# Performance work log

Hardware: AMD Instinct MI355X
Metric: run time of the kernel (lower is better)

The kernel has to match this reference:

```python
import jax, jax.numpy as jnp
import numpy as np

DIM = 1024
HEADS = 16


def setup_inputs() -> dict:
    key = jax.random.key(0)
    ks = jax.random.split(key, 9)
    B, N, C = 2, 2048, DIM
    hd = C // HEADS
    s = 1.0 / np.sqrt(C)
    x = jax.random.normal(ks[0], (B, N, C), dtype=jnp.float32)
    wq = jax.random.normal(ks[1], (C, C), dtype=jnp.float32) * s
    wk = jax.random.normal(ks[2], (C, C), dtype=jnp.float32) * s
    wv = jax.random.normal(ks[3], (C, C), dtype=jnp.float32) * s
    wp = jax.random.normal(ks[4], (C, C), dtype=jnp.float32) * s
    bp = jnp.zeros((C,), dtype=jnp.float32)
    # rotary table: angles theta_j = 10000^{-2j/hd}, positions 0..N-1
    inv_freq = 1.0 / (10000.0 ** (jnp.arange(0, hd, 2, dtype=jnp.float32) / hd))
    ang = jnp.arange(N, dtype=jnp.float32)[:, None] * inv_freq[None, :]  # (N, hd//2)
    cos = jnp.cos(ang)
    sin = jnp.sin(ang)
    return {"x": x, "wq": wq, "wk": wk, "wv": wv, "wp": wp, "bp": bp,
            "cos": cos, "sin": sin, "num_heads": HEADS}


def _apply_rotary(t, cos, sin):
    # t: (B, N, H, D); cos/sin: (N, D//2) -> broadcast (1, N, 1, D//2)
    B, N, H, D = t.shape
    tr = t.reshape(B, N, H, D // 2, 2)
    t1, t2 = tr[..., 0], tr[..., 1]
    c = cos[None, :, None, :]
    s = sin[None, :, None, :]
    o1 = t1 * c - t2 * s
    o2 = t1 * s + t2 * c
    return jnp.stack([o1, o2], axis=-1).reshape(B, N, H, D)


def reference(x, wq, wk, wv, wp, bp, cos, sin, num_heads):
    B, N, C = x.shape
    H = num_heads
    D = C // H
    q = (x @ wq.T).reshape(B, N, H, D)
    k = (x @ wk.T).reshape(B, N, H, D)
    v = (x @ wv.T).reshape(B, N, H, D)
    q = _apply_rotary(q, cos, sin)
    k = _apply_rotary(k, cos, sin)
    scale = 1.0 / jnp.sqrt(jnp.asarray(D, dtype=x.dtype))
    # scores: (B, H, N, N)
    scores = jnp.einsum('bnhd,bmhd->bhnm', q, k) * scale
    attn = jax.nn.softmax(scores, axis=-1)
    out = jnp.einsum('bhnm,bmhd->bnhd', attn, v).reshape(B, N, C)
    return out @ wp.T + bp
```

## Files before the change

### kernel.cpp

```cpp
#include <hip/hip_runtime.h>
#include <hip/hip_bf16.h>
#include <stdint.h>

#define DEVI __device__ __forceinline__

using bf16 = __hip_bfloat16;
typedef __bf16 bf16x8 __attribute__((ext_vector_type(8)));
typedef __bf16 bf16x4 __attribute__((ext_vector_type(4)));
typedef float f32x4 __attribute__((ext_vector_type(4)));

static constexpr int Bb = 2, Nn = 2048, Cc = 1024, Hh = 16, Dd = 64;
static constexpr float CSC = 0.125f * 1.44269504088896340736f;

DEVI bf16 f2bf(float x) {
  __bf16 h = (__bf16)x;
  return *(bf16*)&h;
}
DEVI float fexp2(float x) { return __builtin_amdgcn_exp2f(x); }

DEVI bf16x8 cvt8(f32x4 a, f32x4 b) {
  bf16x8 r;
  r[0] = (__bf16)a[0]; r[1] = (__bf16)a[1]; r[2] = (__bf16)a[2]; r[3] = (__bf16)a[3];
  r[4] = (__bf16)b[0]; r[5] = (__bf16)b[1]; r[6] = (__bf16)b[2]; r[7] = (__bf16)b[3];
  return r;
}

DEVI void gld_lds16(const bf16* g, bf16* l) {
  __builtin_amdgcn_global_load_lds(
      (__attribute__((address_space(1))) void*)(g),
      (__attribute__((address_space(3))) void*)(l),
      16, 0, 0);
}

__global__ __launch_bounds__(256) void k_cvt(const float* __restrict__ x,
                                             const float* __restrict__ wq,
                                             const float* __restrict__ wk,
                                             const float* __restrict__ wv,
                                             const float* __restrict__ wp,
                                             bf16* xb, bf16* wqb, bf16* wkb,
                                             bf16* wvb, bf16* wpb) {
  int bid = blockIdx.x;
  const float* src; bf16* dst; size_t off;
  if (bid < 2048) {
    src = x; dst = xb; off = (size_t)bid * 2048;
  } else {
    int s = (bid - 2048) >> 9, r = (bid - 2048) & 511;
    off = (size_t)r * 2048;
    src = s == 0 ? wq : s == 1 ? wk : s == 2 ? wv : wp;
    dst = s == 0 ? wqb : s == 1 ? wkb : s == 2 ? wvb : wpb;
  }
  size_t i = off + (size_t)threadIdx.x * 8;
  f32x4 a = *(const f32x4*)(src + i);
  f32x4 b = *(const f32x4*)(src + i + 4);
  *(bf16x8*)(dst + i) = cvt8(a, b);
}

template <int MFC, class Epi>
DEVI void gemm_lds_body(const bf16* __restrict__ A, const bf16* __restrict__ Bw,
                        int K, int m0, int n0, bf16* lA, bf16* lB, Epi epi) {
  constexpr int BM = MFC * 32;
  constexpr int PA = BM / 32;
  const int t = threadIdx.x;
  const int lane = t & 63, wave = t >> 6;
  const int wr = wave >> 1, wc = wave & 1;

  f32x4 acc[MFC][4] = {};

  for (int k0 = 0; k0 < K; k0 += 64) {
    __syncthreads();
#pragma unroll
    for (int p = 0; p < PA; ++p) {
      int c = p * 256 + t;
      int row = c >> 3, cis = (c & 7) ^ (row & 7);
      gld_lds16(A + (size_t)(m0 + row) * K + k0 + cis * 8,
                lA + (size_t)(p * 256 + wave * 64) * 8);
    }
#pragma unroll
    for (int p = 0; p < 4; ++p) {
      int c = p * 256 + t;
      int row = c >> 3, cis = (c & 7) ^ (row & 7);
      gld_lds16(Bw + (size_t)(n0 + row) * K + k0 + cis * 8,
                lB + (size_t)(p * 256 + wave * 64) * 8);
    }
    __syncthreads();

#pragma unroll
    for (int kk = 0; kk < 2; ++kk) {
      bf16x8 aF[MFC];
#pragma unroll
      for (int mf = 0; mf < MFC; ++mf) {
        int row = wr * (BM / 2) + mf * 16 + (lane & 15);
        aF[mf] = *(const bf16x8*)(lA + ((row * 64 + kk * 32 + (lane >> 4) * 8) ^ ((row & 7) << 3)));
      }
#pragma unroll
      for (int nf = 0; nf < 4; ++nf) {
        int row = wc * 64 + nf * 16 + (lane & 15);
        bf16x8 bF = *(const bf16x8*)(lB + ((row * 64 + kk * 32 + (lane >> 4) * 8) ^ ((row & 7) << 3)));
#pragma unroll
        for (int mf = 0; mf < MFC; ++mf)
          acc[mf][nf] = __builtin_amdgcn_mfma_f32_16x16x32_bf16(aF[mf], bF, acc[mf][nf], 0, 0, 0);
      }
    }
  }

#pragma unroll
  for (int mf = 0; mf < MFC; ++mf)
#pragma unroll
    for (int nf = 0; nf < 4; ++nf)
#pragma unroll
      for (int r = 0; r < 4; ++r) {
        int gm = m0 + wr * (BM / 2) + mf * 16 + (lane >> 4) * 4 + r;
        int gn = n0 + wc * 64 + nf * 16 + (lane & 15);
        epi(gm, gn, acc[mf][nf][r]);
      }
}

struct EpiRope {
  bf16* dst; const float* cosw; const float* sinw; float scale;
  DEVI void operator()(int gm, int gn, float v) const {
    int b = gm >> 11, n = gm & 2047;
    int h = gn >> 6, d = gn & 63;
    int i = d >> 1;
    float c = cosw[n * 32 + i], s = sinw[n * 32 + i];
    float p = __shfl_xor(v, 1);
    float o = (d & 1) ? (p * s + v * c) : (v * c - p * s);
    dst[((size_t)(b * Hh + h) * Nn + n) * 64 + d] = f2bf(o * scale);
  }
};

struct EpiVt {
  bf16* dst;
  DEVI void operator()(int gm, int gn, float v) const {
    int h = gm >> 6, d = gm & 63;
    int b = gn >> 11, n = gn & 2047;
    dst[((size_t)(b * Hh + h) * 64 + d) * Nn + n] = f2bf(v);
  }
};

struct EpiProj {
  float* dst; const float* bias;
  DEVI void operator()(int gm, int gn, float v) const {
    dst[(size_t)gm * Cc + gn] = v + bias[gn];
  }
};

__global__ __launch_bounds__(256) void k_qkv(const bf16* __restrict__ xb,
                                             const bf16* __restrict__ wqb,
                                             const bf16* __restrict__ wkb,
                                             const bf16* __restrict__ wvb,
                                             bf16* q_ws, bf16* k_ws, bf16* vt_ws,
                                             const float* __restrict__ cw,
                                             const float* __restrict__ sw) {
  __shared__ __align__(16) bf16 smem[2 * 128 * 64];
  bf16* lA = smem;
  bf16* lB = smem + 128 * 64;
  int bid = blockIdx.x;
  if (bid < 512) {
    int sub = bid & 255;
    int m0 = (sub >> 3) * 128, n0 = (sub & 7) * 128;
    bool isq = bid < 256;
    gemm_lds_body<4>(xb, isq ? wqb : wkb, Cc, m0, n0, lA, lB,
                     EpiRope{isq ? q_ws : k_ws, cw, sw, isq ? CSC : 1.0f});
  } else {
    int sub = bid - 512;
    int m0 = (sub & 7) * 128, n0 = (sub >> 3) * 128;
    gemm_lds_body<4>(wvb, xb, Cc, m0, n0, lA, lB, EpiVt{vt_ws});
  }
}

__global__ __launch_bounds__(256) void k_proj(const bf16* __restrict__ A,
                                              const bf16* __restrict__ W,
                                              float* dst, const float* __restrict__ bias) {
  __shared__ __align__(16) bf16 smem[64 * 64 + 128 * 64];
  gemm_lds_body<2>(A, W, Cc, blockIdx.x * 64, blockIdx.y * 128,
                   smem, smem + 64 * 64, EpiProj{dst, bias});
}

__global__ __launch_bounds__(256) void k_flash(const bf16* __restrict__ q_ws,
                                               const bf16* __restrict__ k_ws,
                                               const bf16* __restrict__ vt_ws,
                                               bf16* __restrict__ attn_o) {
  __shared__ __align__(16) bf16 lK[2][64 * 64];
  __shared__ __align__(16) bf16 lV[2][64 * 64];
  __shared__ __align__(16) bf16 pbuf[4][32 * 64];

  const int t = threadIdx.x, lane = t & 63, wave = t >> 6;
  const int g = lane >> 4;
  const int bh = blockIdx.y;
  const int q0 = blockIdx.x * 128 + wave * 32;
  const bf16* qg = q_ws + (size_t)bh * Nn * 64;
  const bf16* kg = k_ws + (size_t)bh * Nn * 64;
  const bf16* vg = vt_ws + (size_t)bh * 64 * Nn;

  bf16x8 qF[2][2];
#pragma unroll
  for (int qs = 0; qs < 2; ++qs)
#pragma unroll
    for (int kd = 0; kd < 2; ++kd)
      qF[qs][kd] = *(const bf16x8*)(qg + (size_t)(q0 + qs * 16 + (lane & 15)) * 64 + kd * 32 + g * 8);

  f32x4 accO[2][4] = {};
  float LsL[2] = {0.f, 0.f};

  auto stage_tile = [&](int kt, int buf) {
#pragma unroll
    for (int p = 0; p < 2; ++p) {
      int c = p * 256 + t;
      int row = c >> 3, cis = (c & 7) ^ (row & 7);
      bf16* dst = (bf16*)((p * 256 + wave * 64) * 8);
      gld_lds16(kg + (size_t)(kt * 64 + row) * 64 + cis * 8,
                lK[buf] + (size_t)(p * 256 + wave * 64) * 8);
      gld_lds16(vg + (size_t)row * Nn + kt * 64 + cis * 8,
                lV[buf] + (size_t)(p * 256 + wave * 64) * 8);
      (void)dst;
    }
  };

  stage_tile(0, 0);
  __syncthreads();

  constexpr int NT = Nn / 64;
  for (int kt = 0; kt < NT; ++kt) {
    const int cur = kt & 1;
    if (kt + 1 < NT) stage_tile(kt + 1, cur ^ 1);

    f32x4 accT[2][4];
    __builtin_amdgcn_s_setprio(1);
#pragma unroll
    for (int nf = 0; nf < 4; ++nf) {
      int row = nf * 16 + (lane & 15);
      bf16x8 kF0 = *(const bf16x8*)(lK[cur] + ((row * 64 + 0 * 32 + g * 8) ^ ((row & 7) << 3)));
      bf16x8 kF1 = *(const bf16x8*)(lK[cur] + ((row * 64 + 1 * 32 + g * 8) ^ ((row & 7) << 3)));
#pragma unroll
      for (int qs = 0; qs < 2; ++qs) {
        f32x4 sacc = {};
        sacc = __builtin_amdgcn_mfma_f32_16x16x32_bf16(kF0, qF[qs][0], sacc, 0, 0, 0);
        sacc = __builtin_amdgcn_mfma_f32_16x16x32_bf16(kF1, qF[qs][1], sacc, 0, 0, 0);
        accT[qs][nf] = sacc;
      }
    }
    __builtin_amdgcn_s_setprio(0);

#pragma unroll
    for (int qs = 0; qs < 2; ++qs) {
      int prow = qs * 16 + (lane & 15);
      float ps = 0.f;
#pragma unroll
      for (int nf = 0; nf < 4; ++nf) {
        bf16x4 pk;
#pragma unroll
        for (int r = 0; r < 4; ++r) {
          float pv = fexp2(accT[qs][nf][r]);
          ps += pv;
          pk[r] = (__bf16)pv;
        }
        int idx = (prow * 64 + nf * 16 + g * 4) ^ ((prow & 7) << 3);
        *(bf16x4*)(pbuf[wave] + idx) = pk;
      }
      LsL[qs] += ps;
    }

    __builtin_amdgcn_s_setprio(1);
#pragma unroll
    for (int kd = 0; kd < 2; ++kd) {
      bf16x8 pF[2];
#pragma unroll
      for (int qs = 0; qs < 2; ++qs) {
        int prow = qs * 16 + (lane & 15);
        pF[qs] = *(const bf16x8*)(pbuf[wave] + ((prow * 64 + kd * 32 + g * 8) ^ ((prow & 7) << 3)));
      }
#pragma unroll
      for (int nf = 0; nf < 4; ++nf) {
        int row = nf * 16 + (lane & 15);
        bf16x8 vF = *(const bf16x8*)(lV[cur] + ((row * 64 + kd * 32 + g * 8) ^ ((row & 7) << 3)));
#pragma unroll
        for (int qs = 0; qs < 2; ++qs)
          accO[qs][nf] = __builtin_amdgcn_mfma_f32_16x16x32_bf16(pF[qs], vF, accO[qs][nf], 0, 0, 0);
      }
    }
    __builtin_amdgcn_s_setprio(0);

    __syncthreads();
  }

  float Lq[2];
#pragma unroll
  for (int qs = 0; qs < 2; ++qs) {
    float s = LsL[qs];
    s += __shfl_xor(s, 16);
    s += __shfl_xor(s, 32);
    Lq[qs] = s;
  }

  const int b = bh >> 4, h = bh & 15;
#pragma unroll
  for (int qs = 0; qs < 2; ++qs)
#pragma unroll
    for (int r = 0; r < 4; ++r) {
      float inv = 1.0f / __shfl(Lq[qs], g * 4 + r);
      int qrow = q0 + qs * 16 + g * 4 + r;
#pragma unroll
      for (int nf = 0; nf < 4; ++nf) {
        int d = nf * 16 + (lane & 15);
        attn_o[((size_t)(b * Nn + qrow)) * Cc + h * 64 + d] = f2bf(accO[qs][nf][r] * inv);
      }
    }
}

extern "C" void kernel_launch(void* const* d_in, const int* in_sizes, int n_in,
                              void* d_out, int out_size, void* d_ws, size_t ws_size,
                              hipStream_t stream) {
  (void)in_sizes; (void)n_in; (void)out_size; (void)ws_size;
  const float* x  = (const float*)d_in[0];
  const float* wq = (const float*)d_in[1];
  const float* wk = (const float*)d_in[2];
  const float* wv = (const float*)d_in[3];
  const float* wp = (const float*)d_in[4];
  const float* bp = (const float*)d_in[5];
  const float* cw = (const float*)d_in[6];
  const float* sw = (const float*)d_in[7];
  float* out = (float*)d_out;

  const size_t M1 = 1u << 20;
  bf16* x_bf  = (bf16*)d_ws;
  bf16* wq_bf = x_bf + 4 * M1;
  bf16* wk_bf = wq_bf + M1;
  bf16* wv_bf = wk_bf + M1;
  bf16* wp_bf = wv_bf + M1;
  bf16* q_ws  = wp_bf + M1;
  bf16* k_ws  = q_ws + 4 * M1;
  bf16* vt_ws = k_ws + 4 * M1;
  bf16* ao_ws = x_bf;

  k_cvt  <<<dim3(4096),    dim3(256), 0, stream>>>(x, wq, wk, wv, wp,
                                                   x_bf, wq_bf, wk_bf, wv_bf, wp_bf);
  k_qkv  <<<dim3(768),     dim3(256), 0, stream>>>(x_bf, wq_bf, wk_bf, wv_bf,
                                                   q_ws, k_ws, vt_ws, cw, sw);
  k_flash<<<dim3(16, 32),  dim3(256), 0, stream>>>(q_ws, k_ws, vt_ws, ao_ws);
  k_proj <<<dim3(64, 8),   dim3(256), 0, stream>>>(ao_ws, wp_bf, out, bp);
}
```

Baseline: 134.2 us.

## Double-buffer GEMM LDS staging with 32-wide K slices and no swizzle

Rewrites the shared GEMM body used by the QKV and projection kernels. It now double-buffers LDS tiles, prefetching the next K slice while computing on the current one, so global-to-LDS loads overlap with MFMA work. The K step drops from 64 to 32 so the two buffers fit in roughly the same LDS, and the XOR swizzle is removed. The trade-off is twice as many barriers per K, less MFMA work per stage, and possible LDS bank conflicts now that rows are 64-byte strided without swizzling.

```diff
diff --git a/kernel.cpp b/kernel.cpp
--- a/kernel.cpp
+++ b/kernel.cpp
@@ -56,51 +56,53 @@
 }
 
 template <int MFC, class Epi>
-DEVI void gemm_lds_body(const bf16* __restrict__ A, const bf16* __restrict__ Bw,
-                        int K, int m0, int n0, bf16* lA, bf16* lB, Epi epi) {
+DEVI void gemm_dbuf(const bf16* __restrict__ A, const bf16* __restrict__ Bw,
+                    int K, int m0, int n0, bf16* lA, bf16* lB, Epi epi) {
   constexpr int BM = MFC * 32;
-  constexpr int PA = BM / 32;
+  constexpr int PA = BM / 64;
+  constexpr int ASZ = BM * 32, BSZ = 128 * 32;
   const int t = threadIdx.x;
-  const int lane = t & 63, wave = t >> 6;
+  const int lane = t & 63, wave = t >> 6, g = lane >> 4;
   const int wr = wave >> 1, wc = wave & 1;
 
-  f32x4 acc[MFC][4] = {};
-
-  for (int k0 = 0; k0 < K; k0 += 64) {
-    __syncthreads();
+  auto stage = [&](int k0, int buf) {
 #pragma unroll
     for (int p = 0; p < PA; ++p) {
       int c = p * 256 + t;
-      int row = c >> 3, cis = (c & 7) ^ (row & 7);
-      gld_lds16(A + (size_t)(m0 + row) * K + k0 + cis * 8,
-                lA + (size_t)(p * 256 + wave * 64) * 8);
-    }
-#pragma unroll
-    for (int p = 0; p < 4; ++p) {
+      gld_lds16(A + (size_t)(m0 + (c >> 2)) * K + k0 + (c & 3) * 8,
+                lA + buf * ASZ + (size_t)(p * 256 + wave * 64) * 8);
+    }
+#pragma unroll
+    for (int p = 0; p < 2; ++p) {
       int c = p * 256 + t;
-      int row = c >> 3, cis = (c & 7) ^ (row & 7);
-      gld_lds16(Bw + (size_t)(n0 + row) * K + k0 + cis * 8,
-                lB + (size_t)(p * 256 + wave * 64) * 8);
+      gld_lds16(Bw + (size_t)(n0 + (c >> 2)) * K + k0 + (c & 3) * 8,
+                lB + buf * BSZ + (size_t)(p * 256 + wave * 64) * 8);
+    }
+  };
+
+  f32x4 acc[MFC][4] = {};
+  stage(0, 0);
+  __syncthreads();
+
+  const int NS = K / 32;
+  for (int s = 0; s < NS; ++s) {
+    const int cur = s & 1;
+    if (s + 1 < NS) stage((s + 1) * 32, cur ^ 1);
+
+    bf16x8 aF[MFC];
+#pragma unroll
+    for (int mf = 0; mf < MFC; ++mf)
+      aF[mf] = *(const bf16x8*)(lA + cur * ASZ +
+                                (wr * (BM / 2) + mf * 16 + (lane & 15)) * 32 + g * 8);
+#pragma unroll
+    for (int nf = 0; nf < 4; ++nf) {
+      bf16x8 bF = *(const bf16x8*)(lB + cur * BSZ +
+                                   (wc * 64 + nf * 16 + (lane & 15)) * 32 + g * 8);
+#pragma unroll
+      for (int mf = 0; mf < MFC; ++mf)
+        acc[mf][nf] = __builtin_amdgcn_mfma_f32_16x16x32_bf16(aF[mf], bF, acc[mf][nf], 0, 0, 0);
     }
     __syncthreads();
-
-#pragma unroll
-    for (int kk = 0; kk < 2; ++kk) {
-      bf16x8 aF[MFC];
-#pragma unroll
-      for (int mf = 0; mf < MFC; ++mf) {
-        int row = wr * (BM / 2) + mf * 16 + (lane & 15);
-        aF[mf] = *(const bf16x8*)(lA + ((row * 64 + kk * 32 + (lane >> 4) * 8) ^ ((row & 7) << 3)));
-      }
-#pragma unroll
-      for (int nf = 0; nf < 4; ++nf) {
-        int row = wc * 64 + nf * 16 + (lane & 15);
-        bf16x8 bF = *(const bf16x8*)(lB + ((row * 64 + kk * 32 + (lane >> 4) * 8) ^ ((row & 7) << 3)));
-#pragma unroll
-        for (int mf = 0; mf < MFC; ++mf)
-          acc[mf][nf] = __builtin_amdgcn_mfma_f32_16x16x32_bf16(aF[mf], bF, acc[mf][nf], 0, 0, 0);
-      }
-    }
   }
 
 #pragma unroll
@@ -109,7 +111,7 @@
     for (int nf = 0; nf < 4; ++nf)
 #pragma unroll
       for (int r = 0; r < 4; ++r) {
-        int gm = m0 + wr * (BM / 2) + mf * 16 + (lane >> 4) * 4 + r;
+        int gm = m0 + wr * (BM / 2) + mf * 16 + g * 4 + r;
         int gn = n0 + wc * 64 + nf * 16 + (lane & 15);
         epi(gm, gn, acc[mf][nf][r]);
       }
@@ -151,29 +153,29 @@
                                              bf16* q_ws, bf16* k_ws, bf16* vt_ws,
                                              const float* __restrict__ cw,
                                              const float* __restrict__ sw) {
-  __shared__ __align__(16) bf16 smem[2 * 128 * 64];
-  bf16* lA = smem;
-  bf16* lB = smem + 128 * 64;
+  __shared__ __align__(16) bf16 lA[2 * 128 * 32];
+  __shared__ __align__(16) bf16 lB[2 * 128 * 32];
   int bid = blockIdx.x;
   if (bid < 512) {
     int sub = bid & 255;
     int m0 = (sub >> 3) * 128, n0 = (sub & 7) * 128;
     bool isq = bid < 256;
-    gemm_lds_body<4>(xb, isq ? wqb : wkb, Cc, m0, n0, lA, lB,
-                     EpiRope{isq ? q_ws : k_ws, cw, sw, isq ? CSC : 1.0f});
+    gemm_dbuf<4>(xb, isq ? wqb : wkb, Cc, m0, n0, lA, lB,
+                 EpiRope{isq ? q_ws : k_ws, cw, sw, isq ? CSC : 1.0f});
   } else {
     int sub = bid - 512;
     int m0 = (sub & 7) * 128, n0 = (sub >> 3) * 128;
-    gemm_lds_body<4>(wvb, xb, Cc, m0, n0, lA, lB, EpiVt{vt_ws});
+    gemm_dbuf<4>(wvb, xb, Cc, m0, n0, lA, lB, EpiVt{vt_ws});
   }
 }
 
 __global__ __launch_bounds__(256) void k_proj(const bf16* __restrict__ A,
                                               const bf16* __restrict__ W,
                                               float* dst, const float* __restrict__ bias) {
-  __shared__ __align__(16) bf16 smem[64 * 64 + 128 * 64];
-  gemm_lds_body<2>(A, W, Cc, blockIdx.x * 64, blockIdx.y * 128,
-                   smem, smem + 64 * 64, EpiProj{dst, bias});
+  __shared__ __align__(16) bf16 lA[2 * 64 * 32];
+  __shared__ __align__(16) bf16 lB[2 * 128 * 32];
+  gemm_dbuf<2>(A, W, Cc, blockIdx.x * 64, blockIdx.y * 128, lA, lB,
+               EpiProj{dst, bias});
 }
 
 __global__ __launch_bounds__(256) void k_flash(const bf16* __restrict__ q_ws,
@@ -207,12 +209,10 @@
     for (int p = 0; p < 2; ++p) {
       int c = p * 256 + t;
       int row = c >> 3, cis = (c & 7) ^ (row & 7);
-      bf16* dst = (bf16*)((p * 256 + wave * 64) * 8);
       gld_lds16(kg + (size_t)(kt * 64 + row) * 64 + cis * 8,
                 lK[buf] + (size_t)(p * 256 + wave * 64) * 8);
       gld_lds16(vg + (size_t)row * Nn + kt * 64 + cis * 8,
                 lV[buf] + (size_t)(p * 256 + wave * 64) * 8);
-      (void)dst;
     }
   };
 
```

Result: faster. 130.1 us (-3.0%).

## Halve GEMM K-step, drop LDS swizzle, and remap block IDs for XCD locality

Applied to the files above, without the earlier changes.

The shared GEMM body now stages a 32-wide K slice per iteration instead of 64 and drops the XOR swizzle. This halves LDS use per block, which may allow more resident blocks, but doubles the number of barriers and risks LDS bank conflicts on the unswizzled fragment reads. The QKV and flash kernels get new block-index mappings so that consecutive block IDs, which are spread round-robin across XCDs, share weight or head data in each XCD's L2. The flash launch becomes a flat 1D grid to support this remapping.

```diff
diff --git a/kernel.cpp b/kernel.cpp
--- a/kernel.cpp
+++ b/kernel.cpp
@@ -12,10 +12,7 @@
 static constexpr int Bb = 2, Nn = 2048, Cc = 1024, Hh = 16, Dd = 64;
 static constexpr float CSC = 0.125f * 1.44269504088896340736f;
 
-DEVI bf16 f2bf(float x) {
-  __bf16 h = (__bf16)x;
-  return *(bf16*)&h;
-}
+DEVI bf16 f2bf(float x) { __bf16 h = (__bf16)x; return *(bf16*)&h; }
 DEVI float fexp2(float x) { return __builtin_amdgcn_exp2f(x); }
 
 DEVI bf16x8 cvt8(f32x4 a, f32x4 b) {
@@ -59,47 +56,41 @@
 DEVI void gemm_lds_body(const bf16* __restrict__ A, const bf16* __restrict__ Bw,
                         int K, int m0, int n0, bf16* lA, bf16* lB, Epi epi) {
   constexpr int BM = MFC * 32;
-  constexpr int PA = BM / 32;
+  constexpr int PA = BM / 64;
   const int t = threadIdx.x;
   const int lane = t & 63, wave = t >> 6;
   const int wr = wave >> 1, wc = wave & 1;
 
   f32x4 acc[MFC][4] = {};
 
-  for (int k0 = 0; k0 < K; k0 += 64) {
+  for (int k0 = 0; k0 < K; k0 += 32) {
     __syncthreads();
 #pragma unroll
     for (int p = 0; p < PA; ++p) {
       int c = p * 256 + t;
-      int row = c >> 3, cis = (c & 7) ^ (row & 7);
-      gld_lds16(A + (size_t)(m0 + row) * K + k0 + cis * 8,
+      int row = c >> 2, col = (c & 3) * 8;
+      gld_lds16(A + (size_t)(m0 + row) * K + k0 + col,
                 lA + (size_t)(p * 256 + wave * 64) * 8);
     }
 #pragma unroll
-    for (int p = 0; p < 4; ++p) {
+    for (int p = 0; p < 2; ++p) {
       int c = p * 256 + t;
-      int row = c >> 3, cis = (c & 7) ^ (row & 7);
-      gld_lds16(Bw + (size_t)(n0 + row) * K + k0 + cis * 8,
+      int row = c >> 2, col = (c & 3) * 8;
+      gld_lds16(Bw + (size_t)(n0 + row) * K + k0 + col,
                 lB + (size_t)(p * 256 + wave * 64) * 8);
     }
     __syncthreads();
 
-#pragma unroll
-    for (int kk = 0; kk < 2; ++kk) {
-      bf16x8 aF[MFC];
-#pragma unroll
-      for (int mf = 0; mf < MFC; ++mf) {
-        int row = wr * (BM / 2) + mf * 16 + (lane & 15);
-        aF[mf] = *(const bf16x8*)(lA + ((row * 64 + kk * 32 + (lane >> 4) * 8) ^ ((row & 7) << 3)));
-      }
-#pragma unroll
-      for (int nf = 0; nf < 4; ++nf) {
-        int row = wc * 64 + nf * 16 + (lane & 15);
-        bf16x8 bF = *(const bf16x8*)(lB + ((row * 64 + kk * 32 + (lane >> 4) * 8) ^ ((row & 7) << 3)));
-#pragma unroll
-        for (int mf = 0; mf < MFC; ++mf)
-          acc[mf][nf] = __builtin_amdgcn_mfma_f32_16x16x32_bf16(aF[mf], bF, acc[mf][nf], 0, 0, 0);
-      }
+    bf16x8 aF[MFC];
+#pragma unroll
+    for (int mf = 0; mf < MFC; ++mf)
+      aF[mf] = *(const bf16x8*)(lA + (wr * (BM / 2) + mf * 16 + (lane & 15)) * 32 + (lane >> 4) * 8);
+#pragma unroll
+    for (int nf = 0; nf < 4; ++nf) {
+      bf16x8 bF = *(const bf16x8*)(lB + (wc * 64 + nf * 16 + (lane & 15)) * 32 + (lane >> 4) * 8);
+#pragma unroll
+      for (int mf = 0; mf < MFC; ++mf)
+        acc[mf][nf] = __builtin_amdgcn_mfma_f32_16x16x32_bf16(aF[mf], bF, acc[mf][nf], 0, 0, 0);
     }
   }
 
@@ -151,19 +142,23 @@
                                              bf16* q_ws, bf16* k_ws, bf16* vt_ws,
                                              const float* __restrict__ cw,
                                              const float* __restrict__ sw) {
-  __shared__ __align__(16) bf16 smem[2 * 128 * 64];
+  __shared__ __align__(16) bf16 smem[256 * 32];
   bf16* lA = smem;
-  bf16* lB = smem + 128 * 64;
+  bf16* lB = smem + 128 * 32;
   int bid = blockIdx.x;
   if (bid < 512) {
     int sub = bid & 255;
-    int m0 = (sub >> 3) * 128, n0 = (sub & 7) * 128;
+    int c = sub & 7, rest = sub >> 3;
+    int m0 = (c + 8 * (rest & 3)) * 128;
+    int n0 = (rest >> 2) * 128;
     bool isq = bid < 256;
     gemm_lds_body<4>(xb, isq ? wqb : wkb, Cc, m0, n0, lA, lB,
                      EpiRope{isq ? q_ws : k_ws, cw, sw, isq ? CSC : 1.0f});
   } else {
     int sub = bid - 512;
-    int m0 = (sub & 7) * 128, n0 = (sub >> 3) * 128;
+    int c = sub & 7, rest = sub >> 3;
+    int n0 = (c + 8 * (rest & 3)) * 128;
+    int m0 = (rest >> 2) * 128;
     gemm_lds_body<4>(wvb, xb, Cc, m0, n0, lA, lB, EpiVt{vt_ws});
   }
 }
@@ -171,9 +166,9 @@
 __global__ __launch_bounds__(256) void k_proj(const bf16* __restrict__ A,
                                               const bf16* __restrict__ W,
                                               float* dst, const float* __restrict__ bias) {
-  __shared__ __align__(16) bf16 smem[64 * 64 + 128 * 64];
+  __shared__ __align__(16) bf16 smem[192 * 32];
   gemm_lds_body<2>(A, W, Cc, blockIdx.x * 64, blockIdx.y * 128,
-                   smem, smem + 64 * 64, EpiProj{dst, bias});
+                   smem, smem + 64 * 32, EpiProj{dst, bias});
 }
 
 __global__ __launch_bounds__(256) void k_flash(const bf16* __restrict__ q_ws,
@@ -186,8 +181,10 @@
 
   const int t = threadIdx.x, lane = t & 63, wave = t >> 6;
   const int g = lane >> 4;
-  const int bh = blockIdx.y;
-  const int q0 = blockIdx.x * 128 + wave * 32;
+  const int bid = blockIdx.x;
+  const int slot = bid >> 3;
+  const int bh = (bid & 7) * 4 + (slot >> 4);
+  const int q0 = (slot & 15) * 128 + wave * 32;
   const bf16* qg = q_ws + (size_t)bh * Nn * 64;
   const bf16* kg = k_ws + (size_t)bh * Nn * 64;
   const bf16* vg = vt_ws + (size_t)bh * 64 * Nn;
@@ -207,12 +204,10 @@
     for (int p = 0; p < 2; ++p) {
       int c = p * 256 + t;
       int row = c >> 3, cis = (c & 7) ^ (row & 7);
-      bf16* dst = (bf16*)((p * 256 + wave * 64) * 8);
       gld_lds16(kg + (size_t)(kt * 64 + row) * 64 + cis * 8,
                 lK[buf] + (size_t)(p * 256 + wave * 64) * 8);
       gld_lds16(vg + (size_t)row * Nn + kt * 64 + cis * 8,
                 lV[buf] + (size_t)(p * 256 + wave * 64) * 8);
-      (void)dst;
     }
   };
 
@@ -336,6 +331,6 @@
                                                    x_bf, wq_bf, wk_bf, wv_bf, wp_bf);
   k_qkv  <<<dim3(768),     dim3(256), 0, stream>>>(x_bf, wq_bf, wk_bf, wv_bf,
                                                    q_ws, k_ws, vt_ws, cw, sw);
-  k_flash<<<dim3(16, 32),  dim3(256), 0, stream>>>(q_ws, k_ws, vt_ws, ao_ws);
+  k_flash<<<dim3(512),     dim3(256), 0, stream>>>(q_ws, k_ws, vt_ws, ao_ws);
   k_proj <<<dim3(64, 8),   dim3(256), 0, stream>>>(ao_ws, wp_bf, out, bp);
 }
```

After: 121.3 us. 9.6% less time.
